# Kernel optimization log

Measured on AMD Instinct MI355X. Metric: run time of the kernel, lower is better.

Reference implementation:

```python
import jax, jax.numpy as jnp
import numpy as np

NUM_FIELDS = 26

def setup_inputs() -> dict:
    key = jax.random.key(0)
    ks = jax.random.split(key, 8)
    B, F, D, V, d, af = 4096, NUM_FIELDS, 13, 100000, 64, 64
    return {
        "sparse_feat": jax.random.randint(ks[0], (B, F), 0, V, dtype=jnp.int32),
        "dense_feat": jax.random.uniform(ks[1], (B, D), dtype=jnp.float32),
        "embed_table": jax.random.normal(ks[2], (V, d), dtype=jnp.float32) * 0.05,
        "lin_table": jax.random.normal(ks[3], (V,), dtype=jnp.float32) * 0.05,
        "w_dense": jax.random.normal(ks[4], (D,), dtype=jnp.float32) * 0.1,
        "bias": jnp.zeros((1,), dtype=jnp.float32),
        "W1": jax.random.normal(ks[5], (d, af), dtype=jnp.float32) * (1.0 / np.sqrt(d)),
        "b1": jnp.zeros((af,), dtype=jnp.float32),
        "w2": jax.random.normal(ks[6], (af,), dtype=jnp.float32) * (1.0 / np.sqrt(af)),
        "p": jax.random.normal(ks[7], (d,), dtype=jnp.float32) * (1.0 / np.sqrt(d)),
    }

def reference(sparse_feat, dense_feat, embed_table, lin_table, w_dense, bias, W1, b1, w2, p):
    # Embedding lookup: [B, F, d]
    emb = embed_table[sparse_feat]
    # Linear part: per-field scalar weights + dense linear + bias -> [B]
    linear_out = lin_table[sparse_feat].sum(axis=1) + dense_feat @ w_dense + bias[0]
    # Pairwise interactions i<j (static indices): [B, P, d]
    i_idx, j_idx = np.triu_indices(NUM_FIELDS, k=1)
    att_x = emb[:, i_idx, :] * emb[:, j_idx, :]
    # Attention MLP: Linear(d, af) + ReLU + Linear(af, 1, no bias) -> [B, P]
    h = jax.nn.relu(jnp.einsum('bpd,da->bpa', att_x, W1) + b1)
    att_w = jnp.einsum('bpa,a->bp', h, w2)
    att_score = jax.nn.softmax(att_w, axis=1)
    # Softmax-weighted sum over pairs -> [B, d], then final projection p -> [B]
    att_out = jnp.einsum('bpd,bp->bd', att_x, att_score)
    fm_att_out = att_out @ p
    return linear_out + fm_att_out
```

## Files before the change

kernel.cpp:

```cpp
#include <hip/hip_runtime.h>
#include <math.h>


#define NF 26
#define NP 325
#define NPP 336
#define NMT 21
#define ED 64
#define AF 64
#define NDENSE 13
#define BLOCK 128
#define ESTRIDE 72

typedef __attribute__((ext_vector_type(8))) _Float16 half8;
typedef __attribute__((ext_vector_type(4))) _Float16 half4;
typedef __attribute__((ext_vector_type(4))) float f32x4;

__global__ void prep_kernel(const float* __restrict__ W1,
                            _Float16* __restrict__ w1t,
                            unsigned short* __restrict__ tab)
{
    int t = threadIdx.x;
    for (int idx = t; idx < ED * AF; idx += 256) {
        int d = idx >> 6, a = idx & 63;
        w1t[a * ED + d] = (_Float16)W1[idx];
    }
    if (t < NPP) {
        unsigned short v = 0;
        if (t < NP) {
            int rem = t, i = 0;
            while (rem >= NF - 1 - i) { rem -= NF - 1 - i; ++i; }
            v = (unsigned short)(i | ((i + 1 + rem) << 8));
        }
        tab[t] = v;
    }
}

__global__ __launch_bounds__(BLOCK, 4)
void afm_kernel(const int*   __restrict__ sparse,
                const float* __restrict__ dense,
                const float* __restrict__ etab,
                const float* __restrict__ ltab,
                const float* __restrict__ wdense,
                const float* __restrict__ bias,
                const float* __restrict__ b1,
                const float* __restrict__ w2,
                const float* __restrict__ proj,
                const _Float16* __restrict__ w1t,
                const unsigned short* __restrict__ tab,
                float*       __restrict__ out)
{
    const int t    = threadIdx.x;
    const int wave = t >> 6;
    const int lane = t & 63;
    const int qd   = lane >> 4;
    const int ln   = lane & 15;
    const int r    = blockIdx.x;

    __shared__ alignas(16) _Float16 emb[NF][ESTRIDE];
    __shared__ alignas(16) float    scores[NPP];
    __shared__ alignas(16) float    partial[2][ED];

    half8 bfr[4][2];
    #pragma unroll
    for (int nt = 0; nt < 4; ++nt)
        #pragma unroll
        for (int kh = 0; kh < 2; ++kh)
            bfr[nt][kh] = *(const half8*)(w1t + (nt * 16 + ln) * ED + kh * 32 + qd * 8);

    float b1v[4], w2v[4];
    #pragma unroll
    for (int nt = 0; nt < 4; ++nt) {
        b1v[nt] = b1[nt * 16 + ln];
        w2v[nt] = w2[nt * 16 + ln];
    }

    const int* __restrict__ srow = sparse + r * NF;
    for (int task = t; task < NF * 16; task += BLOCK) {
        int f = task >> 4, q = task & 15;
        float4 v = *(const float4*)(etab + (size_t)srow[f] * ED + q * 4);
        half4 h = { (_Float16)v.x, (_Float16)v.y, (_Float16)v.z, (_Float16)v.w };
        *(half4*)(&emb[f][q * 4]) = h;
    }

    float lin = 0.f;
    if (wave == 0) {
        if (lane < NF) {
            lin = ltab[srow[lane]];
        } else if (lane >= 32 && lane < 32 + NDENSE) {
            int k = lane - 32;
            lin = dense[r * NDENSE + k] * wdense[k];
        }
        #pragma unroll
        for (int off = 32; off >= 1; off >>= 1) lin += __shfl_xor(lin, off, 64);
        lin += bias[0];
    }

    __syncthreads();

    for (int mt = wave; mt < NMT; mt += 2) {
        const int p0 = mt * 16 + ln;
        const unsigned pp = tab[p0];
        const int fi = pp & 0xff, fj = pp >> 8;

        half8 a0 = *(const half8*)(&emb[fi][qd * 8])      * *(const half8*)(&emb[fj][qd * 8]);
        half8 a1 = *(const half8*)(&emb[fi][32 + qd * 8]) * *(const half8*)(&emb[fj][32 + qd * 8]);

        float lg[4] = {0.f, 0.f, 0.f, 0.f};
        #pragma unroll
        for (int nt = 0; nt < 4; ++nt) {
            f32x4 acc = {0.f, 0.f, 0.f, 0.f};
            acc = __builtin_amdgcn_mfma_f32_16x16x32_f16(a0, bfr[nt][0], acc, 0, 0, 0);
            acc = __builtin_amdgcn_mfma_f32_16x16x32_f16(a1, bfr[nt][1], acc, 0, 0, 0);
            #pragma unroll
            for (int rr = 0; rr < 4; ++rr)
                lg[rr] = fmaf(fmaxf(acc[rr] + b1v[nt], 0.f), w2v[nt], lg[rr]);
        }
        #pragma unroll
        for (int off = 1; off <= 8; off <<= 1) {
            #pragma unroll
            for (int rr = 0; rr < 4; ++rr) lg[rr] += __shfl_xor(lg[rr], off, 64);
        }
        if (ln == 0) {
            const int pr = mt * 16 + qd * 4;
            float4 st;
            st.x = (pr + 0 < NP) ? lg[0] : -INFINITY;
            st.y = (pr + 1 < NP) ? lg[1] : -INFINITY;
            st.z = (pr + 2 < NP) ? lg[2] : -INFINITY;
            st.w = (pr + 3 < NP) ? lg[3] : -INFINITY;
            *(float4*)(&scores[pr]) = st;
        }
    }

    __syncthreads();

    float v[6];
    #pragma unroll
    for (int k = 0; k < 6; ++k) {
        int p = lane + (k << 6);
        v[k] = (p < NPP) ? scores[p] : -INFINITY;
    }
    float m = v[0];
    #pragma unroll
    for (int k = 1; k < 6; ++k) m = fmaxf(m, v[k]);
    #pragma unroll
    for (int off = 32; off >= 1; off >>= 1) m = fmaxf(m, __shfl_xor(m, off, 64));
    float e[6], esum = 0.f;
    #pragma unroll
    for (int k = 0; k < 6; ++k) { e[k] = __expf(v[k] - m); esum += e[k]; }
    #pragma unroll
    for (int off = 32; off >= 1; off >>= 1) esum += __shfl_xor(esum, off, 64);
    const float rinv = 1.0f / esum;
    __syncthreads();
    #pragma unroll
    for (int k = 0; k < 6; ++k) {
        if ((k >= wave * 3) && (k < wave * 3 + 3)) {
            int p = lane + (k << 6);
            if (p < NPP) scores[p] = e[k] * rinv;
        }
    }

    __syncthreads();

    const int dg  = lane & 7;
    const int sub = (wave << 3) + (lane >> 3);
    half8 acc8 = { (_Float16)0.f, (_Float16)0.f, (_Float16)0.f, (_Float16)0.f,
                   (_Float16)0.f, (_Float16)0.f, (_Float16)0.f, (_Float16)0.f };
    for (int it = 0; it < NPP / 16; ++it) {
        const int p = it * 16 + sub;
        const float s = scores[p];
        const unsigned pp = tab[p];
        const int fi = pp & 0xff, fj = pp >> 8;
        const _Float16 sh = (_Float16)s;
        half8 sv = { sh, sh, sh, sh, sh, sh, sh, sh };
        half8 x = *(const half8*)(&emb[fi][dg * 8]) * *(const half8*)(&emb[fj][dg * 8]);
        acc8 += sv * x;
    }
    float av[8];
    #pragma unroll
    for (int i = 0; i < 8; ++i) av[i] = (float)acc8[i];
    #pragma unroll
    for (int off = 8; off <= 32; off <<= 1) {
        #pragma unroll
        for (int i = 0; i < 8; ++i) av[i] += __shfl_xor(av[i], off, 64);
    }
    if (lane < 8) {
        *(float4*)(&partial[wave][lane * 8])     = make_float4(av[0], av[1], av[2], av[3]);
        *(float4*)(&partial[wave][lane * 8 + 4]) = make_float4(av[4], av[5], av[6], av[7]);
    }
    __syncthreads();

    if (wave == 0 && lane < 8) {
        float4 s0 = *(const float4*)(&partial[0][lane * 8]);
        float4 s1 = *(const float4*)(&partial[0][lane * 8 + 4]);
        float4 t0 = *(const float4*)(&partial[1][lane * 8]);
        float4 t1 = *(const float4*)(&partial[1][lane * 8 + 4]);
        float4 pa = *(const float4*)(proj + lane * 8);
        float4 pb = *(const float4*)(proj + lane * 8 + 4);
        float part = (s0.x + t0.x) * pa.x + (s0.y + t0.y) * pa.y
                   + (s0.z + t0.z) * pa.z + (s0.w + t0.w) * pa.w
                   + (s1.x + t1.x) * pb.x + (s1.y + t1.y) * pb.y
                   + (s1.z + t1.z) * pb.z + (s1.w + t1.w) * pb.w;
        #pragma unroll
        for (int off = 1; off <= 4; off <<= 1) part += __shfl_xor(part, off, 64);
        if (lane == 0) out[r] = lin + part;
    }
}

extern "C" void kernel_launch(void* const* d_in, const int* in_sizes, int n_in,
                              void* d_out, int out_size, void* d_ws, size_t ws_size,
                              hipStream_t stream) {
    const int*   sparse = (const int*)  d_in[0];
    const float* dense  = (const float*)d_in[1];
    const float* etab   = (const float*)d_in[2];
    const float* ltab   = (const float*)d_in[3];
    const float* wdense = (const float*)d_in[4];
    const float* bias   = (const float*)d_in[5];
    const float* W1     = (const float*)d_in[6];
    const float* b1     = (const float*)d_in[7];
    const float* w2     = (const float*)d_in[8];
    const float* proj   = (const float*)d_in[9];
    float* outp = (float*)d_out;

    _Float16*       w1t = (_Float16*)d_ws;
    unsigned short* tab = (unsigned short*)((char*)d_ws + 8192);

    const int B = in_sizes[0] / NF;

    prep_kernel<<<dim3(1), dim3(256), 0, stream>>>(W1, w1t, tab);
    afm_kernel<<<dim3(B), dim3(BLOCK), 0, stream>>>(
        sparse, dense, etab, ltab, wdense, bias, b1, w2, proj, w1t, tab, outp);
    (void)n_in; (void)out_size; (void)ws_size;
}
```

Measured before the change: 135.2 us.

## Transpose MFMA operands, fold bias into accumulator, pack half reductions

Swaps the MFMA operand order so each lane holds the hidden units for a single pair. The attention logit then needs only two cross-lane shuffles instead of sixteen, and b1 is preloaded as the accumulator initial value. The embedding gather now converts 8 floats per task, and softmax reads and writes scores as float4. The final d-reduction shuffles packed half8 values and projects per wave before a two-value sum, which removes the partial shared buffer. This cuts shuffle and LDS traffic, but the cross-lane sums are now done in fp16, which may lose precision.

```diff
diff --git a/kernel.cpp b/kernel.cpp
--- a/kernel.cpp
+++ b/kernel.cpp
@@ -13,8 +13,14 @@
 #define ESTRIDE 72
 
 typedef __attribute__((ext_vector_type(8))) _Float16 half8;
-typedef __attribute__((ext_vector_type(4))) _Float16 half4;
 typedef __attribute__((ext_vector_type(4))) float f32x4;
+
+__device__ __forceinline__ half8 shfl_xor_h8(half8 v, int off) {
+    union { half8 h; int i[4]; } u; u.h = v;
+    #pragma unroll
+    for (int k = 0; k < 4; ++k) u.i[k] = __shfl_xor(u.i[k], off, 64);
+    return u.h;
+}
 
 __global__ void prep_kernel(const float* __restrict__ W1,
                             _Float16* __restrict__ w1t,
@@ -59,7 +65,7 @@
 
     __shared__ alignas(16) _Float16 emb[NF][ESTRIDE];
     __shared__ alignas(16) float    scores[NPP];
-    __shared__ alignas(16) float    partial[2][ED];
+    __shared__ float pw[2];
 
     half8 bfr[4][2];
     #pragma unroll
@@ -68,19 +74,22 @@
         for (int kh = 0; kh < 2; ++kh)
             bfr[nt][kh] = *(const half8*)(w1t + (nt * 16 + ln) * ED + kh * 32 + qd * 8);
 
-    float b1v[4], w2v[4];
+    float4 b1v4[4], w2v4[4];
     #pragma unroll
     for (int nt = 0; nt < 4; ++nt) {
-        b1v[nt] = b1[nt * 16 + ln];
-        w2v[nt] = w2[nt * 16 + ln];
+        b1v4[nt] = *(const float4*)(b1 + nt * 16 + qd * 4);
+        w2v4[nt] = *(const float4*)(w2 + nt * 16 + qd * 4);
     }
 
     const int* __restrict__ srow = sparse + r * NF;
-    for (int task = t; task < NF * 16; task += BLOCK) {
-        int f = task >> 4, q = task & 15;
-        float4 v = *(const float4*)(etab + (size_t)srow[f] * ED + q * 4);
-        half4 h = { (_Float16)v.x, (_Float16)v.y, (_Float16)v.z, (_Float16)v.w };
-        *(half4*)(&emb[f][q * 4]) = h;
+    for (int task = t; task < NF * 8; task += BLOCK) {
+        int f = task >> 3, c = task & 7;
+        const float* src = etab + (size_t)srow[f] * ED + c * 8;
+        float4 v0 = *(const float4*)(src);
+        float4 v1 = *(const float4*)(src + 4);
+        half8 h = { (_Float16)v0.x, (_Float16)v0.y, (_Float16)v0.z, (_Float16)v0.w,
+                    (_Float16)v1.x, (_Float16)v1.y, (_Float16)v1.z, (_Float16)v1.w };
+        *(half8*)(&emb[f][c * 8]) = h;
     }
 
     float lin = 0.f;
@@ -103,61 +112,52 @@
         const unsigned pp = tab[p0];
         const int fi = pp & 0xff, fj = pp >> 8;
 
-        half8 a0 = *(const half8*)(&emb[fi][qd * 8])      * *(const half8*)(&emb[fj][qd * 8]);
-        half8 a1 = *(const half8*)(&emb[fi][32 + qd * 8]) * *(const half8*)(&emb[fj][32 + qd * 8]);
-
-        float lg[4] = {0.f, 0.f, 0.f, 0.f};
+        half8 x0 = *(const half8*)(&emb[fi][qd * 8])      * *(const half8*)(&emb[fj][qd * 8]);
+        half8 x1 = *(const half8*)(&emb[fi][32 + qd * 8]) * *(const half8*)(&emb[fj][32 + qd * 8]);
+
+        float lg = 0.f;
         #pragma unroll
         for (int nt = 0; nt < 4; ++nt) {
-            f32x4 acc = {0.f, 0.f, 0.f, 0.f};
-            acc = __builtin_amdgcn_mfma_f32_16x16x32_f16(a0, bfr[nt][0], acc, 0, 0, 0);
-            acc = __builtin_amdgcn_mfma_f32_16x16x32_f16(a1, bfr[nt][1], acc, 0, 0, 0);
-            #pragma unroll
-            for (int rr = 0; rr < 4; ++rr)
-                lg[rr] = fmaf(fmaxf(acc[rr] + b1v[nt], 0.f), w2v[nt], lg[rr]);
+            f32x4 acc = { b1v4[nt].x, b1v4[nt].y, b1v4[nt].z, b1v4[nt].w };
+            acc = __builtin_amdgcn_mfma_f32_16x16x32_f16(bfr[nt][0], x0, acc, 0, 0, 0);
+            acc = __builtin_amdgcn_mfma_f32_16x16x32_f16(bfr[nt][1], x1, acc, 0, 0, 0);
+            lg = fmaf(fmaxf(acc[0], 0.f), w2v4[nt].x, lg);
+            lg = fmaf(fmaxf(acc[1], 0.f), w2v4[nt].y, lg);
+            lg = fmaf(fmaxf(acc[2], 0.f), w2v4[nt].z, lg);
+            lg = fmaf(fmaxf(acc[3], 0.f), w2v4[nt].w, lg);
         }
-        #pragma unroll
-        for (int off = 1; off <= 8; off <<= 1) {
-            #pragma unroll
-            for (int rr = 0; rr < 4; ++rr) lg[rr] += __shfl_xor(lg[rr], off, 64);
-        }
-        if (ln == 0) {
-            const int pr = mt * 16 + qd * 4;
-            float4 st;
-            st.x = (pr + 0 < NP) ? lg[0] : -INFINITY;
-            st.y = (pr + 1 < NP) ? lg[1] : -INFINITY;
-            st.z = (pr + 2 < NP) ? lg[2] : -INFINITY;
-            st.w = (pr + 3 < NP) ? lg[3] : -INFINITY;
-            *(float4*)(&scores[pr]) = st;
-        }
-    }
-
-    __syncthreads();
-
-    float v[6];
-    #pragma unroll
-    for (int k = 0; k < 6; ++k) {
-        int p = lane + (k << 6);
-        v[k] = (p < NPP) ? scores[p] : -INFINITY;
-    }
-    float m = v[0];
-    #pragma unroll
-    for (int k = 1; k < 6; ++k) m = fmaxf(m, v[k]);
+        lg += __shfl_xor(lg, 16, 64);
+        lg += __shfl_xor(lg, 32, 64);
+        if (qd == 0) scores[p0] = (p0 < NP) ? lg : -INFINITY;
+    }
+
+    __syncthreads();
+
+    float4 v0 = *(const float4*)(&scores[lane * 4]);
+    float4 v1 = make_float4(-INFINITY, -INFINITY, -INFINITY, -INFINITY);
+    if (lane < NPP / 4 - 64) v1 = *(const float4*)(&scores[(lane + 64) * 4]);
+
+    float m = fmaxf(fmaxf(fmaxf(v0.x, v0.y), fmaxf(v0.z, v0.w)),
+                    fmaxf(fmaxf(v1.x, v1.y), fmaxf(v1.z, v1.w)));
     #pragma unroll
     for (int off = 32; off >= 1; off >>= 1) m = fmaxf(m, __shfl_xor(m, off, 64));
-    float e[6], esum = 0.f;
-    #pragma unroll
-    for (int k = 0; k < 6; ++k) { e[k] = __expf(v[k] - m); esum += e[k]; }
+    float4 e0, e1;
+    e0.x = __expf(v0.x - m); e0.y = __expf(v0.y - m);
+    e0.z = __expf(v0.z - m); e0.w = __expf(v0.w - m);
+    e1.x = __expf(v1.x - m); e1.y = __expf(v1.y - m);
+    e1.z = __expf(v1.z - m); e1.w = __expf(v1.w - m);
+    float esum = e0.x + e0.y + e0.z + e0.w + e1.x + e1.y + e1.z + e1.w;
     #pragma unroll
     for (int off = 32; off >= 1; off >>= 1) esum += __shfl_xor(esum, off, 64);
     const float rinv = 1.0f / esum;
-    __syncthreads();
-    #pragma unroll
-    for (int k = 0; k < 6; ++k) {
-        if ((k >= wave * 3) && (k < wave * 3 + 3)) {
-            int p = lane + (k << 6);
-            if (p < NPP) scores[p] = e[k] * rinv;
-        }
+
+    __syncthreads();
+    if (wave == 0) {
+        e0.x *= rinv; e0.y *= rinv; e0.z *= rinv; e0.w *= rinv;
+        *(float4*)(&scores[lane * 4]) = e0;
+    } else if (lane < NPP / 4 - 64) {
+        e1.x *= rinv; e1.y *= rinv; e1.z *= rinv; e1.w *= rinv;
+        *(float4*)(&scores[(lane + 64) * 4]) = e1;
     }
 
     __syncthreads();
@@ -176,35 +176,21 @@
         half8 x = *(const half8*)(&emb[fi][dg * 8]) * *(const half8*)(&emb[fj][dg * 8]);
         acc8 += sv * x;
     }
-    float av[8];
-    #pragma unroll
-    for (int i = 0; i < 8; ++i) av[i] = (float)acc8[i];
-    #pragma unroll
-    for (int off = 8; off <= 32; off <<= 1) {
-        #pragma unroll
-        for (int i = 0; i < 8; ++i) av[i] += __shfl_xor(av[i], off, 64);
-    }
-    if (lane < 8) {
-        *(float4*)(&partial[wave][lane * 8])     = make_float4(av[0], av[1], av[2], av[3]);
-        *(float4*)(&partial[wave][lane * 8 + 4]) = make_float4(av[4], av[5], av[6], av[7]);
-    }
-    __syncthreads();
-
-    if (wave == 0 && lane < 8) {
-        float4 s0 = *(const float4*)(&partial[0][lane * 8]);
-        float4 s1 = *(const float4*)(&partial[0][lane * 8 + 4]);
-        float4 t0 = *(const float4*)(&partial[1][lane * 8]);
-        float4 t1 = *(const float4*)(&partial[1][lane * 8 + 4]);
-        float4 pa = *(const float4*)(proj + lane * 8);
-        float4 pb = *(const float4*)(proj + lane * 8 + 4);
-        float part = (s0.x + t0.x) * pa.x + (s0.y + t0.y) * pa.y
-                   + (s0.z + t0.z) * pa.z + (s0.w + t0.w) * pa.w
-                   + (s1.x + t1.x) * pb.x + (s1.y + t1.y) * pb.y
-                   + (s1.z + t1.z) * pb.z + (s1.w + t1.w) * pb.w;
-        #pragma unroll
-        for (int off = 1; off <= 4; off <<= 1) part += __shfl_xor(part, off, 64);
-        if (lane == 0) out[r] = lin + part;
-    }
+    acc8 += shfl_xor_h8(acc8, 8);
+    acc8 += shfl_xor_h8(acc8, 16);
+    acc8 += shfl_xor_h8(acc8, 32);
+    float4 pa = *(const float4*)(proj + dg * 8);
+    float4 pb = *(const float4*)(proj + dg * 8 + 4);
+    float part = (float)acc8[0] * pa.x + (float)acc8[1] * pa.y
+               + (float)acc8[2] * pa.z + (float)acc8[3] * pa.w
+               + (float)acc8[4] * pb.x + (float)acc8[5] * pb.y
+               + (float)acc8[6] * pb.z + (float)acc8[7] * pb.w;
+    #pragma unroll
+    for (int off = 1; off <= 4; off <<= 1) part += __shfl_xor(part, off, 64);
+    if (lane == 0) pw[wave] = part;
+
+    __syncthreads();
+    if (t == 0) out[r] = lin + pw[0] + pw[1];
 }
 
 extern "C" void kernel_launch(void* const* d_in, const int* in_sizes, int n_in,
```

Result: faster. 125.5 us (-7.2%).
